# Optimization experiments

Hardware: AMD Instinct MI355X
Metric: run time of the kernel (lower is better)

## Reference

```python
import jax, jax.numpy as jnp
import numpy as np

HEADS = 8
DIM_HEAD = 64

def setup_inputs() -> dict:
    key = jax.random.key(0)
    k1, k2 = jax.random.split(key)
    x = jax.random.normal(k1, (4, 2048, 512), dtype=jnp.float32)
    W_qkv = jax.random.normal(k2, (512, 3 * HEADS * DIM_HEAD), dtype=jnp.float32) * (512 ** -0.5)
    return {"x": x, "W_qkv": W_qkv}

def reference(x, W_qkv):
    b, n, _ = x.shape
    h, d = HEADS, DIM_HEAD
    scale = d ** -0.5
    qkv = x @ W_qkv                                   # [b, n, 3*h*d]
    q, k, v = jnp.split(qkv, 3, axis=-1)
    # 'b n (h d) -> b h n d'
    q = q.reshape(b, n, h, d).transpose(0, 2, 1, 3)
    k = k.reshape(b, n, h, d).transpose(0, 2, 1, 3)
    v = v.reshape(b, n, h, d).transpose(0, 2, 1, 3)
    scores = jnp.einsum('bhid,bhjd->bhij', q, k) * scale
    attn_w = jax.nn.softmax(scores, axis=-1)
    out = jnp.einsum('bhij,bhjd->bhid', attn_w, v)
    # 'b h i d -> b i (h d)'
    return out.transpose(0, 2, 1, 3).reshape(b, n, h * d)
```

## Files before the change

kernel.cpp:

```cpp
#include <hip/hip_runtime.h>

#define BATCH 4
#define NSEQ  2048
#define DMODEL 512
#define NHEAD 8
#define DHEAD 64
#define NQKV  1536

typedef __bf16 bf16x8 __attribute__((ext_vector_type(8)));
typedef __bf16 bf16x4 __attribute__((ext_vector_type(4)));
typedef float  f32x4  __attribute__((ext_vector_type(4)));
typedef short  s16x4  __attribute__((ext_vector_type(4)));

__device__ inline void async16(const __bf16* g, __bf16* l) {
    __builtin_amdgcn_global_load_lds(
        (const __attribute__((address_space(1))) void*)g,
        (__attribute__((address_space(3))) void*)l, 16, 0, 0);
}

__device__ inline bf16x8 cvt8(const float* __restrict__ p) {
    float4 a = *(const float4*)p;
    float4 b = *(const float4*)(p + 4);
    bf16x8 r;
    r[0] = (__bf16)a.x; r[1] = (__bf16)a.y; r[2] = (__bf16)a.z; r[3] = (__bf16)a.w;
    r[4] = (__bf16)b.x; r[5] = (__bf16)b.y; r[6] = (__bf16)b.z; r[7] = (__bf16)b.w;
    return r;
}

__device__ inline f32x4 mfma_pv(s16x4 a, s16x4 b, f32x4 c) {
#if !defined(__HIP_DEVICE_COMPILE__)
    (void)a; (void)b;
    return c;
#elif __has_builtin(__builtin_amdgcn_mfma_f32_16x16x16bf16_1k)
    return __builtin_amdgcn_mfma_f32_16x16x16bf16_1k(a, b, c, 0, 0, 0);
#else
    bf16x4 a4 = __builtin_bit_cast(bf16x4, a);
    bf16x4 b4 = __builtin_bit_cast(bf16x4, b);
    bf16x8 a8 = {}, b8 = {};
    for (int i = 0; i < 4; ++i) { a8[i] = a4[i]; b8[i] = b4[i]; }
    return __builtin_amdgcn_mfma_f32_16x16x32_bf16(a8, b8, c, 0, 0, 0);
#endif
}

#define QSCALE 0.18033688011112042f

__global__ __launch_bounds__(256) void prep_kernel(
    const float* __restrict__ W, __bf16* __restrict__ Wt) {
    __shared__ __bf16 t[64][65];
    const int tid = threadIdx.x;
    const int bi = blockIdx.x;
    const int n0 = (bi % 24) * 64, k0 = (bi / 24) * 64;
    const int cr = tid >> 4;
    const int cc = (tid & 15) * 4;
    for (int p = 0; p < 4; ++p) {
        int r = p * 16 + cr;
        float4 v = *(const float4*)&W[(size_t)(k0 + r) * NQKV + n0 + cc];
        t[r][cc + 0] = (__bf16)v.x; t[r][cc + 1] = (__bf16)v.y;
        t[r][cc + 2] = (__bf16)v.z; t[r][cc + 3] = (__bf16)v.w;
    }
    __syncthreads();
    for (int p = 0; p < 4; ++p) {
        int r = p * 16 + cr;
        bf16x4 o = {t[cc + 0][r], t[cc + 1][r], t[cc + 2][r], t[cc + 3][r]};
        *(bf16x4*)&Wt[(size_t)(n0 + r) * DMODEL + k0 + cc] = o;
    }
}

__global__ __launch_bounds__(512) void qkv_gemm_kernel(
    const float* __restrict__ x, const __bf16* __restrict__ Wt,
    __bf16* __restrict__ Qw, __bf16* __restrict__ Kw, __bf16* __restrict__ Vw) {
    __shared__ __align__(16) char smem[49152];
    __bf16* Al = (__bf16*)smem;
    __bf16* Bl = Al + 16384;
    __bf16* T  = (__bf16*)smem;

    const int tid  = threadIdx.x;
    const int w    = tid >> 6;
    const int lane = tid & 63;
    const int quad = lane >> 4;
    const int l15  = lane & 15;
    const int wm   = w >> 1, wn = w & 1;
    const int m0 = blockIdx.x * 256;
    const int n0 = blockIdx.y * 128;
    const int segrow = lane >> 3;
    const int sc = (lane & 7) ^ segrow;

    f32x4 acc[4][4];
    for (int i = 0; i < 4; ++i)
        for (int j = 0; j < 4; ++j)
            acc[i][j] = (f32x4){0.f, 0.f, 0.f, 0.f};

    for (int kt = 0; kt < 8; ++kt) {
        const int k0 = kt * 64;
        for (int i = 0; i < 2; ++i) {
            int seg = w * 2 + i;
            int row = seg * 8 + segrow;
            async16(&Wt[(size_t)(n0 + row) * DMODEL + k0 + sc * 8], &Bl[seg * 512]);
        }
        bf16x8 avs[4];
        int aoff[4];
        for (int p = 0; p < 4; ++p) {
            int g = p * 512 + tid;
            int row = g >> 3, ch = g & 7;
            avs[p] = cvt8(&x[(size_t)(m0 + row) * DMODEL + k0 + ch * 8]);
            aoff[p] = (row >> 3) * 512 + ((row & 7) * 8 + (ch ^ (row & 7))) * 8;
        }
        for (int p = 0; p < 4; ++p)
            *(bf16x8*)&Al[aoff[p]] = avs[p];
        __syncthreads();
        for (int kc = 0; kc < 2; ++kc) {
            bf16x8 af[4], bfr[4];
            for (int mb = 0; mb < 4; ++mb) {
                int row = wm * 64 + mb * 16 + l15;
                af[mb] = *(const bf16x8*)&Al[(row >> 3) * 512 +
                    ((row & 7) * 8 + ((kc * 4 + quad) ^ (row & 7))) * 8];
            }
            for (int nb = 0; nb < 4; ++nb) {
                int row = wn * 64 + nb * 16 + l15;
                bfr[nb] = *(const bf16x8*)&Bl[row * 64 + (((kc * 4 + quad) ^ (l15 & 7)) * 8)];
            }
            for (int mb = 0; mb < 4; ++mb)
                for (int nb = 0; nb < 4; ++nb)
                    acc[mb][nb] = __builtin_amdgcn_mfma_f32_16x16x32_bf16(
                        af[mb], bfr[nb], acc[mb][nb], 0, 0, 0);
        }
        __syncthreads();
    }

    const int which = n0 >> 9;
    const int bb  = m0 >> 11;
    const int nq0 = m0 & 2047;

    for (int ph = 0; ph < 2; ++ph) {
        if (which <= 1) {
            if ((wm >> 1) == ph)
                for (int mb = 0; mb < 4; ++mb)
                    for (int nb = 0; nb < 4; ++nb)
                        for (int r = 0; r < 4; ++r) {
                            int ml = (wm & 1) * 64 + mb * 16 + quad * 4 + r;
                            int nl = wn * 64 + nb * 16 + l15;
                            float a = acc[mb][nb][r];
                            if (which == 0) a *= QSCALE;
                            T[ml * 136 + nl] = (__bf16)a;
                        }
            __syncthreads();
            __bf16* dst = which ? Kw : Qw;
            const int h0 = (n0 & 511) >> 6;
            const int region = tid >> 8;
            const int bh = bb * NHEAD + h0 + region;
            __bf16* base = dst + ((size_t)bh * NSEQ + nq0 + ph * 128) * DHEAD;
            for (int i = 0; i < 4; ++i) {
                int chunk = (tid & 255) + i * 256;
                int f = chunk * 8;
                int ml = f >> 6, dd = f & 63;
                bf16x8 v = *(const bf16x8*)&T[ml * 136 + region * 64 + dd];
                *(bf16x8*)&base[ml * 64 + dd] = v;
            }
        } else {
            if ((wm >> 1) == ph)
                for (int mb = 0; mb < 4; ++mb)
                    for (int nb = 0; nb < 4; ++nb) {
                        int nl = wn * 64 + nb * 16 + l15;
                        int mlb = (wm & 1) * 64 + mb * 16 + quad * 4;
                        bf16x4 v = {(__bf16)acc[mb][nb][0], (__bf16)acc[mb][nb][1],
                                    (__bf16)acc[mb][nb][2], (__bf16)acc[mb][nb][3]};
                        *(bf16x4*)&T[nl * 136 + mlb] = v;
                    }
            __syncthreads();
            const int hv0 = ((n0 - 1024) & 511) >> 6;
            for (int i = 0; i < 4; ++i) {
                int gc = i * 512 + tid;
                int row = gc >> 4, ch = gc & 15;
                bf16x8 v = *(const bf16x8*)&T[row * 136 + ch * 8];
                int bh = bb * NHEAD + hv0 + (row >> 6);
                int dd = row & 63;
                *(bf16x8*)&Vw[((size_t)bh * DHEAD + dd) * NSEQ + nq0 + ph * 128 + ch * 8] = v;
            }
        }
        __syncthreads();
    }
}

__global__ __launch_bounds__(512) void attn_kernel(
    const __bf16* __restrict__ Qw, const __bf16* __restrict__ Kw,
    const __bf16* __restrict__ Vw, float* __restrict__ out) {
    __shared__ __align__(16) char smem[65536];
    float* Of = (float*)smem;

    const int tid  = threadIdx.x;
    const int w    = tid >> 6;
    const int wg   = w & 3;
    const int half = w >> 2;
    const int lane = tid & 63;
    const int quad = lane >> 4;
    const int l15  = lane & 15;
    const int bh = blockIdx.y;
    const int bb = bh >> 3, h = bh & 7;
    const int q0 = blockIdx.x * 128 + wg * 32;
    const int segrow = lane >> 3;
    const int sc = (lane & 7) ^ segrow;

    __bf16* HB = (__bf16*)smem + half * 16384;

    const __bf16* Qh = Qw + (size_t)bh * NSEQ * DHEAD;
    const __bf16* Kh = Kw + (size_t)bh * NSEQ * DHEAD;
    const __bf16* Vh = Vw + (size_t)bh * DHEAD * NSEQ;

    bf16x8 qf[2][2];
    for (int qb = 0; qb < 2; ++qb)
        for (int kc = 0; kc < 2; ++kc)
            qf[qb][kc] = *(const bf16x8*)&Qh[(size_t)(q0 + qb * 16 + l15) * DHEAD + kc * 32 + quad * 8];

    f32x4 O[4][2];
    float l_st[2] = {0.f, 0.f};
    for (int db = 0; db < 4; ++db)
        for (int qb = 0; qb < 2; ++qb)
            O[db][qb] = (f32x4){0.f, 0.f, 0.f, 0.f};

    auto stage = [&](int it, int b) {
        const int k0 = (half * 16 + it) * 64;
        __bf16* KL = HB + b * 8192;
        __bf16* VL = KL + 4096;
        for (int i = 0; i < 2; ++i) {
            int seg = wg * 2 + i;
            int row = seg * 8 + segrow;
            async16(&Kh[(size_t)(k0 + row) * DHEAD + sc * 8], &KL[seg * 512]);
            async16(&Vh[(size_t)row * NSEQ + k0 + sc * 8], &VL[seg * 512]);
        }
    };

    stage(0, 0);
    for (int it = 0; it < 16; ++it) {
        __syncthreads();
        if (it < 15) stage(it + 1, (it + 1) & 1);
        const __bf16* Kb = HB + (it & 1) * 8192;
        const __bf16* Vb = Kb + 4096;

        f32x4 s[4][2];
        for (int kb = 0; kb < 4; ++kb)
            for (int qb = 0; qb < 2; ++qb)
                s[kb][qb] = (f32x4){0.f, 0.f, 0.f, 0.f};
        for (int kc = 0; kc < 2; ++kc) {
            bf16x8 ak[4];
            for (int kb = 0; kb < 4; ++kb) {
                int row = kb * 16 + l15;
                ak[kb] = *(const bf16x8*)&Kb[row * 64 + (((kc * 4 + quad) ^ (l15 & 7)) * 8)];
            }
            for (int kb = 0; kb < 4; ++kb)
                for (int qb = 0; qb < 2; ++qb)
                    s[kb][qb] = __builtin_amdgcn_mfma_f32_16x16x32_bf16(
                        ak[kb], qf[qb][kc], s[kb][qb], 0, 0, 0);
        }

        s16x4 pb[4][2];
        for (int qb = 0; qb < 2; ++qb) {
            float rsum = 0.f;
            for (int kb = 0; kb < 4; ++kb) {
                bf16x4 t;
                for (int r = 0; r < 4; ++r) {
                    float p = __builtin_amdgcn_exp2f(s[kb][qb][r]);
                    rsum += p;
                    t[r] = (__bf16)p;
                }
                pb[kb][qb] = __builtin_bit_cast(s16x4, t);
            }
            l_st[qb] += rsum;
        }

        for (int kb = 0; kb < 4; ++kb) {
            s16x4 av[4];
            for (int db = 0; db < 4; ++db) {
                int d = db * 16 + l15;
                int g = kb * 2 + (quad >> 1);
                av[db] = *(const s16x4*)&Vb[(d >> 3) * 512 + (d & 7) * 64 +
                                            ((g ^ (d & 7)) * 8) + (quad & 1) * 4];
            }
            for (int db = 0; db < 4; ++db)
                for (int qb = 0; qb < 2; ++qb)
                    O[db][qb] = mfma_pv(av[db], pb[kb][qb], O[db][qb]);
        }
    }

    for (int qb = 0; qb < 2; ++qb) {
        l_st[qb] += __shfl_xor(l_st[qb], 16);
        l_st[qb] += __shfl_xor(l_st[qb], 32);
    }

    __syncthreads();
    if (half == 0) {
        for (int qb = 0; qb < 2; ++qb) {
            int q = wg * 32 + qb * 16 + l15;
            for (int db = 0; db < 4; ++db)
                *(f32x4*)&Of[q * 68 + db * 16 + quad * 4] = O[db][qb];
            if (quad == 0) Of[q * 68 + 64] = l_st[qb];
        }
    }
    __syncthreads();
    if (half == 1) {
        for (int qb = 0; qb < 2; ++qb) {
            int q = wg * 32 + qb * 16 + l15;
            float inv = 1.f / (l_st[qb] + Of[q * 68 + 64]);
            for (int db = 0; db < 4; ++db) {
                f32x4 v = *(const f32x4*)&Of[q * 68 + db * 16 + quad * 4];
                v = (v + O[db][qb]) * inv;
                *(f32x4*)&Of[q * 68 + db * 16 + quad * 4] = v;
            }
        }
    }
    __syncthreads();
    const int nqb = blockIdx.x * 128;
    for (int i = 0; i < 4; ++i) {
        int gc = i * 512 + tid;
        int row = gc >> 4, ch = gc & 15;
        f32x4 v = *(const f32x4*)&Of[row * 68 + ch * 4];
        *(f32x4*)&out[((size_t)(bb * NSEQ + nqb + row)) * DMODEL + h * DHEAD + ch * 4] = v;
    }
}

extern "C" void kernel_launch(void* const* d_in, const int* in_sizes, int n_in,
                              void* d_out, int out_size, void* d_ws, size_t ws_size,
                              hipStream_t stream) {
    const float* x = (const float*)d_in[0];
    const float* W = (const float*)d_in[1];
    float* out = (float*)d_out;

    __bf16* wsp = (__bf16*)d_ws;
    __bf16* Wt = wsp;
    __bf16* Qw = Wt + 786432;
    __bf16* Kw = Qw + 4194304;
    __bf16* Vw = Kw + 4194304;

    prep_kernel<<<192, 256, 0, stream>>>(W, Wt);
    qkv_gemm_kernel<<<dim3(32, 12), 512, 0, stream>>>(x, Wt, Qw, Kw, Vw);
    attn_kernel<<<dim3(16, 32), 512, 0, stream>>>(Qw, Kw, Vw, out);
}
```

Before: 139.3 us.

## Switch attention kernel to 32x32x16 bf16 MFMA with lane-shuffled P operand

Rewrites the attention inner loop to use 32x32x16 bf16 MFMA for both QK^T and PV instead of 16x16x32 and 16x16x16 tiles. The P fragment is rebuilt with cross-half-wave shuffles so the S accumulator layout can feed PV directly, and LDS offsets are precomputed per thread. This cuts MFMA instruction count and LDS fragment loads per tile. It also adds a min-blocks hint to launch_bounds, which raises register pressure risk and costs extra shuffles per tile.

Result: slower. 147.3 us (+5.7%).

```diff
diff --git a/kernel.cpp b/kernel.cpp
--- a/kernel.cpp
+++ b/kernel.cpp
@@ -10,7 +10,8 @@
 typedef __bf16 bf16x8 __attribute__((ext_vector_type(8)));
 typedef __bf16 bf16x4 __attribute__((ext_vector_type(4)));
 typedef float  f32x4  __attribute__((ext_vector_type(4)));
-typedef short  s16x4  __attribute__((ext_vector_type(4)));
+typedef float  f32x16 __attribute__((ext_vector_type(16)));
+typedef unsigned int u32x4 __attribute__((ext_vector_type(4)));
 
 __device__ inline void async16(const __bf16* g, __bf16* l) {
     __builtin_amdgcn_global_load_lds(
@@ -25,21 +26,6 @@
     r[0] = (__bf16)a.x; r[1] = (__bf16)a.y; r[2] = (__bf16)a.z; r[3] = (__bf16)a.w;
     r[4] = (__bf16)b.x; r[5] = (__bf16)b.y; r[6] = (__bf16)b.z; r[7] = (__bf16)b.w;
     return r;
-}
-
-__device__ inline f32x4 mfma_pv(s16x4 a, s16x4 b, f32x4 c) {
-#if !defined(__HIP_DEVICE_COMPILE__)
-    (void)a; (void)b;
-    return c;
-#elif __has_builtin(__builtin_amdgcn_mfma_f32_16x16x16bf16_1k)
-    return __builtin_amdgcn_mfma_f32_16x16x16bf16_1k(a, b, c, 0, 0, 0);
-#else
-    bf16x4 a4 = __builtin_bit_cast(bf16x4, a);
-    bf16x4 b4 = __builtin_bit_cast(bf16x4, b);
-    bf16x8 a8 = {}, b8 = {};
-    for (int i = 0; i < 4; ++i) { a8[i] = a4[i]; b8[i] = b4[i]; }
-    return __builtin_amdgcn_mfma_f32_16x16x32_bf16(a8, b8, c, 0, 0, 0);
-#endif
 }
 
 #define QSCALE 0.18033688011112042f
@@ -181,7 +167,7 @@
     }
 }
 
-__global__ __launch_bounds__(512) void attn_kernel(
+__global__ __launch_bounds__(512, 4) void attn_kernel(
     const __bf16* __restrict__ Qw, const __bf16* __restrict__ Kw,
     const __bf16* __restrict__ Vw, float* __restrict__ out) {
     __shared__ __align__(16) char smem[65536];
@@ -192,8 +178,8 @@
     const int wg   = w & 3;
     const int half = w >> 2;
     const int lane = tid & 63;
-    const int quad = lane >> 4;
-    const int l15  = lane & 15;
+    const int cl   = lane & 31;
+    const int b5   = lane >> 5;
     const int bh = blockIdx.y;
     const int bb = bh >> 3, h = bh & 7;
     const int q0 = blockIdx.x * 128 + wg * 32;
@@ -206,16 +192,24 @@
     const __bf16* Kh = Kw + (size_t)bh * NSEQ * DHEAD;
     const __bf16* Vh = Vw + (size_t)bh * DHEAD * NSEQ;
 
-    bf16x8 qf[2][2];
-    for (int qb = 0; qb < 2; ++qb)
-        for (int kc = 0; kc < 2; ++kc)
-            qf[qb][kc] = *(const bf16x8*)&Qh[(size_t)(q0 + qb * 16 + l15) * DHEAD + kc * 32 + quad * 8];
-
-    f32x4 O[4][2];
-    float l_st[2] = {0.f, 0.f};
-    for (int db = 0; db < 4; ++db)
-        for (int qb = 0; qb < 2; ++qb)
-            O[db][qb] = (f32x4){0.f, 0.f, 0.f, 0.f};
+    bf16x8 qf[4];
+#pragma unroll
+    for (int c4 = 0; c4 < 4; ++c4)
+        qf[c4] = *(const bf16x8*)&Qh[(size_t)(q0 + cl) * DHEAD + c4 * 16 + b5 * 8];
+
+    int off[2][4];
+#pragma unroll
+    for (int rt = 0; rt < 2; ++rt)
+#pragma unroll
+        for (int x = 0; x < 4; ++x)
+            off[rt][x] = (rt * 32 + cl) * 64 + (((2 * x + b5) ^ (cl & 7)) * 8);
+
+    f32x16 O[2];
+#pragma unroll
+    for (int dt = 0; dt < 2; ++dt)
+#pragma unroll
+        for (int i = 0; i < 16; ++i) O[dt][i] = 0.f;
+    float l_st = 0.f;
 
     auto stage = [&](int it, int b) {
         const int k0 = (half * 16 + it) * 64;
@@ -236,76 +230,85 @@
         const __bf16* Kb = HB + (it & 1) * 8192;
         const __bf16* Vb = Kb + 4096;
 
-        f32x4 s[4][2];
-        for (int kb = 0; kb < 4; ++kb)
-            for (int qb = 0; qb < 2; ++qb)
-                s[kb][qb] = (f32x4){0.f, 0.f, 0.f, 0.f};
-        for (int kc = 0; kc < 2; ++kc) {
-            bf16x8 ak[4];
-            for (int kb = 0; kb < 4; ++kb) {
-                int row = kb * 16 + l15;
-                ak[kb] = *(const bf16x8*)&Kb[row * 64 + (((kc * 4 + quad) ^ (l15 & 7)) * 8)];
-            }
-            for (int kb = 0; kb < 4; ++kb)
-                for (int qb = 0; qb < 2; ++qb)
-                    s[kb][qb] = __builtin_amdgcn_mfma_f32_16x16x32_bf16(
-                        ak[kb], qf[qb][kc], s[kb][qb], 0, 0, 0);
-        }
-
-        s16x4 pb[4][2];
-        for (int qb = 0; qb < 2; ++qb) {
-            float rsum = 0.f;
-            for (int kb = 0; kb < 4; ++kb) {
-                bf16x4 t;
-                for (int r = 0; r < 4; ++r) {
-                    float p = __builtin_amdgcn_exp2f(s[kb][qb][r]);
-                    rsum += p;
-                    t[r] = (__bf16)p;
+        f32x16 s[2];
+#pragma unroll
+        for (int t = 0; t < 2; ++t)
+#pragma unroll
+            for (int i = 0; i < 16; ++i) s[t][i] = 0.f;
+#pragma unroll
+        for (int c4 = 0; c4 < 4; ++c4) {
+            bf16x8 a0 = *(const bf16x8*)&Kb[off[0][c4]];
+            bf16x8 a1 = *(const bf16x8*)&Kb[off[1][c4]];
+            s[0] = __builtin_amdgcn_mfma_f32_32x32x16_bf16(a0, qf[c4], s[0], 0, 0, 0);
+            s[1] = __builtin_amdgcn_mfma_f32_32x32x16_bf16(a1, qf[c4], s[1], 0, 0, 0);
+        }
+
+        unsigned u[2][4][2];
+        float rsum = 0.f;
+#pragma unroll
+        for (int t = 0; t < 2; ++t)
+#pragma unroll
+            for (int g = 0; g < 4; ++g)
+#pragma unroll
+                for (int p = 0; p < 2; ++p) {
+                    float e0 = __builtin_amdgcn_exp2f(s[t][g * 4 + 2 * p + 0]);
+                    float e1 = __builtin_amdgcn_exp2f(s[t][g * 4 + 2 * p + 1]);
+                    rsum += e0;
+                    rsum += e1;
+                    unsigned short h0 = __builtin_bit_cast(unsigned short, (__bf16)e0);
+                    unsigned short h1 = __builtin_bit_cast(unsigned short, (__bf16)e1);
+                    u[t][g][p] = (unsigned)h0 | ((unsigned)h1 << 16);
                 }
-                pb[kb][qb] = __builtin_bit_cast(s16x4, t);
-            }
-            l_st[qb] += rsum;
-        }
-
-        for (int kb = 0; kb < 4; ++kb) {
-            s16x4 av[4];
-            for (int db = 0; db < 4; ++db) {
-                int d = db * 16 + l15;
-                int g = kb * 2 + (quad >> 1);
-                av[db] = *(const s16x4*)&Vb[(d >> 3) * 512 + (d & 7) * 64 +
-                                            ((g ^ (d & 7)) * 8) + (quad & 1) * 4];
-            }
-            for (int db = 0; db < 4; ++db)
-                for (int qb = 0; qb < 2; ++qb)
-                    O[db][qb] = mfma_pv(av[db], pb[kb][qb], O[db][qb]);
-        }
-    }
-
-    for (int qb = 0; qb < 2; ++qb) {
-        l_st[qb] += __shfl_xor(l_st[qb], 16);
-        l_st[qb] += __shfl_xor(l_st[qb], 32);
-    }
+        l_st += rsum;
+
+#pragma unroll
+        for (int G = 0; G < 4; ++G) {
+            const int t = G >> 1, hh = (G & 1) * 2;
+            u32x4 bw;
+#pragma unroll
+            for (int p = 0; p < 2; ++p) {
+                unsigned d = u[t][hh][p], sv = u[t][hh + 1][p];
+                unsigned dx = __shfl_xor(d, 32);
+                unsigned sx = __shfl_xor(sv, 32);
+                bw[p]     = b5 ? sx : d;
+                bw[2 + p] = b5 ? sv : dx;
+            }
+            bf16x8 pb = __builtin_bit_cast(bf16x8, bw);
+            bf16x8 av0 = *(const bf16x8*)&Vb[off[0][G]];
+            bf16x8 av1 = *(const bf16x8*)&Vb[off[1][G]];
+            O[0] = __builtin_amdgcn_mfma_f32_32x32x16_bf16(av0, pb, O[0], 0, 0, 0);
+            O[1] = __builtin_amdgcn_mfma_f32_32x32x16_bf16(av1, pb, O[1], 0, 0, 0);
+        }
+    }
+
+    l_st += __shfl_xor(l_st, 32);
 
     __syncthreads();
+    const int q = wg * 32 + cl;
     if (half == 0) {
-        for (int qb = 0; qb < 2; ++qb) {
-            int q = wg * 32 + qb * 16 + l15;
-            for (int db = 0; db < 4; ++db)
-                *(f32x4*)&Of[q * 68 + db * 16 + quad * 4] = O[db][qb];
-            if (quad == 0) Of[q * 68 + 64] = l_st[qb];
-        }
+#pragma unroll
+        for (int dt = 0; dt < 2; ++dt)
+#pragma unroll
+            for (int g = 0; g < 4; ++g) {
+                f32x4 v = {O[dt][4 * g + 0], O[dt][4 * g + 1],
+                           O[dt][4 * g + 2], O[dt][4 * g + 3]};
+                *(f32x4*)&Of[q * 68 + dt * 32 + g * 8 + b5 * 4] = v;
+            }
+        if (b5 == 0) Of[q * 68 + 64] = l_st;
     }
     __syncthreads();
     if (half == 1) {
-        for (int qb = 0; qb < 2; ++qb) {
-            int q = wg * 32 + qb * 16 + l15;
-            float inv = 1.f / (l_st[qb] + Of[q * 68 + 64]);
-            for (int db = 0; db < 4; ++db) {
-                f32x4 v = *(const f32x4*)&Of[q * 68 + db * 16 + quad * 4];
-                v = (v + O[db][qb]) * inv;
-                *(f32x4*)&Of[q * 68 + db * 16 + quad * 4] = v;
-            }
-        }
+        float inv = 1.f / (l_st + Of[q * 68 + 64]);
+#pragma unroll
+        for (int dt = 0; dt < 2; ++dt)
+#pragma unroll
+            for (int g = 0; g < 4; ++g) {
+                f32x4 v = *(const f32x4*)&Of[q * 68 + dt * 32 + g * 8 + b5 * 4];
+                f32x4 o = {O[dt][4 * g + 0], O[dt][4 * g + 1],
+                           O[dt][4 * g + 2], O[dt][4 * g + 3]};
+                v = (v + o) * inv;
+                *(f32x4*)&Of[q * 68 + dt * 32 + g * 8 + b5 * 4] = v;
+            }
     }
     __syncthreads();
     const int nqb = blockIdx.x * 128;
```
